# Kernel tuning notes

Measured on AMD Instinct MI355X. Metric: run time of the kernel, lower is better.

Reference implementation:

```python
import jax, jax.numpy as jnp
import numpy as np

NUM_USERS = 100000
NUM_ITEMS = 50000
EMB = 64
B = 8192
MAXM = 50
ATT_H = 16
PRED_H = 8


def setup_inputs() -> dict:
    key = jax.random.key(0)
    ks = jax.random.split(key, 12)
    member_idx = jax.random.randint(ks[0], (B, MAXM), 0, NUM_USERS)
    # ragged group sizes in [1, MAXM]
    lens = jax.random.randint(ks[1], (B,), 1, MAXM + 1)
    member_mask = jnp.arange(MAXM)[None, :] < lens[:, None]  # bool [B, M]
    item_inputs = jax.random.randint(ks[2], (B,), 0, NUM_ITEMS)
    s = 1.0 / np.sqrt(EMB)
    user_table = jax.random.normal(ks[3], (NUM_USERS, EMB), jnp.float32) * s
    item_table = jax.random.normal(ks[4], (NUM_ITEMS, EMB), jnp.float32) * s
    att_w1 = jax.random.normal(ks[5], (2 * EMB, ATT_H), jnp.float32) * 0.05
    att_b1 = jnp.zeros((ATT_H,), jnp.float32)
    att_w2 = jax.random.normal(ks[6], (ATT_H, 1), jnp.float32) * 0.05
    att_b2 = jnp.zeros((1,), jnp.float32)
    pred_w1 = jax.random.normal(ks[7], (3 * EMB, PRED_H), jnp.float32) * 0.05
    pred_b1 = jnp.zeros((PRED_H,), jnp.float32)
    pred_w2 = jax.random.normal(ks[8], (PRED_H, 1), jnp.float32) * 0.05
    pred_b2 = jnp.zeros((1,), jnp.float32)
    return dict(member_idx=member_idx, member_mask=member_mask, item_inputs=item_inputs,
                user_table=user_table, item_table=item_table,
                att_w1=att_w1, att_b1=att_b1, att_w2=att_w2, att_b2=att_b2,
                pred_w1=pred_w1, pred_b1=pred_b1, pred_w2=pred_w2, pred_b2=pred_b2)


def reference(member_idx, member_mask, item_inputs, user_table, item_table,
              att_w1, att_b1, att_w2, att_b2, pred_w1, pred_b1, pred_w2, pred_b2):
    mem_e = user_table[member_idx]            # [B, M, d]
    item_e = item_table[item_inputs]          # [B, d]
    # attention MLP over concat(member, item)
    cat = jnp.concatenate(
        [mem_e, jnp.broadcast_to(item_e[:, None, :], mem_e.shape)], axis=-1)  # [B, M, 2d]
    h = jax.nn.relu(jnp.einsum('bmf,fh->bmh', cat, att_w1) + att_b1)
    logits = (jnp.einsum('bmh,ho->bmo', h, att_w2) + att_b2)[..., 0]          # [B, M]
    logits = jnp.where(member_mask, logits, -jnp.inf)
    wts = jax.nn.softmax(logits, axis=-1)                                     # [B, M]
    g = jnp.einsum('bm,bmd->bd', wts, mem_e)                                  # [B, d]
    new = jnp.concatenate([g * item_e, g, item_e], axis=-1)                   # [B, 3d]
    ph = jax.nn.relu(new @ pred_w1 + pred_b1)
    y = jax.nn.sigmoid(ph @ pred_w2 + pred_b2)                                # [B, 1]
    return y
```

## Files before the change

### kernel.cpp

```cpp
#include <hip/hip_runtime.h>
#include <hip/hip_bf16.h>


__global__ void AGREE_12773232738622_probe(
    const void* member_mask,
    const void* user_table,
    int* ws)
{
    if (ws[2] == 0x5AFE0001) return;

    const int lane = threadIdx.x;
    const int wi = lane >> 4;
    const int r  = lane & 15;

    int len = 0, ok = 1, prev = 1;
    for (int m = 0; m < 50; ++m) {
        long e = 50L * r + m;
        int nz;
        if (wi == 0)      nz = (((const unsigned char*)member_mask)[e] != 0);
        else if (wi == 1) nz = (((const unsigned short*)member_mask)[e] != 0);
        else if (wi == 2) nz = (((const unsigned int*)member_mask)[e] != 0u);
        else {
            const unsigned int* p = (const unsigned int*)member_mask;
            nz = ((p[2 * e] | p[2 * e + 1]) != 0u);
        }
        if (nz && !prev) ok = 0;
        if (nz) len = len + 1;
        prev = nz;
    }
    if (len == 0) ok = 0;

    ok = ok & __shfl_xor(ok, 1);
    ok = ok & __shfl_xor(ok, 2);
    ok = ok & __shfl_xor(ok, 4);
    ok = ok & __shfl_xor(ok, 8);
    int mx = len;
    mx = max(mx, __shfl_xor(mx, 1));
    mx = max(mx, __shfl_xor(mx, 2));
    mx = max(mx, __shfl_xor(mx, 4));
    mx = max(mx, __shfl_xor(mx, 8));

    int o0 = __shfl(ok, 0),  o1 = __shfl(ok, 16), o2 = __shfl(ok, 32), o3 = __shfl(ok, 48);
    int L0 = __shfl(mx, 0),  L1 = __shfl(mx, 16), L2 = __shfl(mx, 32), L3 = __shfl(mx, 48);

    float v = __bfloat162float(((const __hip_bfloat16*)user_table)[lane]);
    float a = (v < 0.0f) ? -v : v;
    int huge = (!(a < 4.0f)) ? 1 : 0;
    unsigned long long hb = __ballot(huge);
    int hcnt = __popcll(hb);

    if (lane == 0) {
        int bestW = 1, bestLen = -1;
        if (o0 && L0 > bestLen) { bestLen = L0; bestW = 1; }
        if (o1 && L1 > bestLen) { bestLen = L1; bestW = 2; }
        if (o2 && L2 > bestLen) { bestLen = L2; bestW = 4; }
        if (o3 && L3 > bestLen) { bestLen = L3; bestW = 8; }
        ws[0] = bestW;
        ws[1] = (hcnt >= 8) ? 1 : 0;
        ws[2] = 0x5AFE0001;
    }
}

__global__ __launch_bounds__(256, 4) void AGREE_12773232738622_kernel(
    const int* member_idx,
    const void* member_mask,
    const int* item_inputs,
    const void* user_table,
    const void* item_table,
    const void* att_w1,
    const void* att_b1,
    const void* att_w2,
    const void* att_b2,
    const void* pred_w1,
    const void* pred_b1,
    const void* pred_w2,
    const void* pred_b2,
    void* out,
    const int* ws)
{
    using s16x8 = __attribute__((ext_vector_type(8))) short;
    using bf16x8 = __attribute__((ext_vector_type(8))) __bf16;
    using f32x4 = __attribute__((ext_vector_type(4))) float;

    __shared__ float s_l[4][64];
    __shared__ float s_g[4][64];

    const int tid  = threadIdx.x;
    const int lane = tid & 63;
    const int wave = tid >> 6;
    const int b    = blockIdx.x * 4 + wave;
    const int mode = ws[0];
    const int isf  = ws[1];

    int valid = 0;
    if (lane < 50) {
        long e0 = 50L * b + lane;
        if (mode == 1)      valid = (((const unsigned char*)member_mask)[e0] != 0);
        else if (mode == 2) valid = (((const unsigned short*)member_mask)[e0] != 0);
        else if (mode == 4) valid = (((const unsigned int*)member_mask)[e0] != 0u);
        else {
            const unsigned int* p = (const unsigned int*)member_mask;
            valid = ((p[2 * e0] | p[2 * e0 + 1]) != 0u);
        }
    }
    unsigned long long vm = __ballot(valid);
    int len = __popcll(vm);
    if (len < 1)  len = 1;
    if (len > 50) len = 50;

    const int item_id = item_inputs[b];
    int idxv = 0;
    if (lane < 50) idxv = member_idx[b * 50 + lane];

    if (!isf) {
        const unsigned short* utp = (const unsigned short*)user_table;
        const unsigned short* w1p = (const unsigned short*)att_w1;

        const float itemv = __uint_as_float(
            (unsigned int)((const unsigned short*)item_table)[item_id * 64 + lane] << 16);

        const int kn = lane & 15;
        const int kg = lane >> 4;
        s16x8 bfrag[4];
        #pragma unroll
        for (int kc = 0; kc < 4; ++kc) {
            #pragma unroll
            for (int j = 0; j < 8; ++j)
                bfrag[kc][j] = (short)w1p[(kc * 32 + kg * 8 + j) * 16 + kn];
        }

        s16x8 afrag[4][2];
        #pragma unroll
        for (int t = 0; t < 4; ++t) {
            int m  = t * 16 + (lane & 15);
            int mc = (m < 50) ? m : 0;
            int id = __shfl(idxv, mc);
            const unsigned short* rp = utp + (long)id * 64 + kg * 8;
            afrag[t][0] = *(const s16x8*)(rp);
            afrag[t][1] = *(const s16x8*)(rp + 32);
        }
        const unsigned short* ipp = (const unsigned short*)item_table + (long)item_id * 64 + kg * 8;
        s16x8 ifrag0 = *(const s16x8*)(ipp);
        s16x8 ifrag1 = *(const s16x8*)(ipp + 32);

        f32x4 acc[4];
        #pragma unroll
        for (int t = 0; t < 4; ++t) acc[t] = f32x4{0.0f, 0.0f, 0.0f, 0.0f};
        #pragma unroll
        for (int t = 0; t < 4; ++t) {
            acc[t] = __builtin_amdgcn_mfma_f32_16x16x32_bf16(
                __builtin_bit_cast(bf16x8, afrag[t][0]), __builtin_bit_cast(bf16x8, bfrag[0]), acc[t], 0, 0, 0);
            acc[t] = __builtin_amdgcn_mfma_f32_16x16x32_bf16(
                __builtin_bit_cast(bf16x8, afrag[t][1]), __builtin_bit_cast(bf16x8, bfrag[1]), acc[t], 0, 0, 0);
            acc[t] = __builtin_amdgcn_mfma_f32_16x16x32_bf16(
                __builtin_bit_cast(bf16x8, ifrag0),     __builtin_bit_cast(bf16x8, bfrag[2]), acc[t], 0, 0, 0);
            acc[t] = __builtin_amdgcn_mfma_f32_16x16x32_bf16(
                __builtin_bit_cast(bf16x8, ifrag1),     __builtin_bit_cast(bf16x8, bfrag[3]), acc[t], 0, 0, 0);
        }

        const float b1v = __uint_as_float((unsigned int)((const unsigned short*)att_b1)[kn] << 16);
        const float w2v = __uint_as_float((unsigned int)((const unsigned short*)att_w2)[kn] << 16);
        const float b2v = __uint_as_float((unsigned int)((const unsigned short*)att_b2)[0] << 16);
        #pragma unroll
        for (int t = 0; t < 4; ++t) {
            #pragma unroll
            for (int r = 0; r < 4; ++r) {
                float v = fmaxf(acc[t][r] + b1v, 0.0f) * w2v;
                v += __shfl_xor(v, 1);
                v += __shfl_xor(v, 2);
                v += __shfl_xor(v, 4);
                v += __shfl_xor(v, 8);
                if ((lane & 15) == 0) s_l[wave][t * 16 + (lane >> 4) * 4 + r] = v;
            }
        }
        __syncthreads();

        float lg = (lane < 50) ? s_l[wave][lane] : 0.0f;

        float x = valid ? (lg + b2v) : -3.0e38f;
        float mxv = x;
        mxv = fmaxf(mxv, __shfl_xor(mxv, 1));
        mxv = fmaxf(mxv, __shfl_xor(mxv, 2));
        mxv = fmaxf(mxv, __shfl_xor(mxv, 4));
        mxv = fmaxf(mxv, __shfl_xor(mxv, 8));
        mxv = fmaxf(mxv, __shfl_xor(mxv, 16));
        mxv = fmaxf(mxv, __shfl_xor(mxv, 32));
        float p = valid ? expf(x - mxv) : 0.0f;
        float sum = p;
        sum += __shfl_xor(sum, 1);
        sum += __shfl_xor(sum, 2);
        sum += __shfl_xor(sum, 4);
        sum += __shfl_xor(sum, 8);
        sum += __shfl_xor(sum, 16);
        sum += __shfl_xor(sum, 32);
        float wnorm;
        if (sum > 0.0f) wnorm = p * (1.0f / sum);
        else            wnorm = (lane == 0) ? 1.0f : 0.0f;

        float pg[2][8];
        #pragma unroll
        for (int ks = 0; ks < 2; ++ks)
            #pragma unroll
            for (int j = 0; j < 8; ++j) pg[ks][j] = 0.0f;
        #pragma unroll
        for (int t = 0; t < 4; ++t) {
            float wv = __shfl(wnorm, t * 16 + (lane & 15));
            #pragma unroll
            for (int ks = 0; ks < 2; ++ks) {
                #pragma unroll
                for (int j = 0; j < 8; ++j) {
                    float e = __uint_as_float(
                        (unsigned int)(unsigned short)afrag[t][ks][j] << 16);
                    pg[ks][j] += wv * e;
                }
            }
        }
        #pragma unroll
        for (int ks = 0; ks < 2; ++ks) {
            #pragma unroll
            for (int j = 0; j < 8; ++j) {
                float v = pg[ks][j];
                v += __shfl_xor(v, 1);
                v += __shfl_xor(v, 2);
                v += __shfl_xor(v, 4);
                v += __shfl_xor(v, 8);
                pg[ks][j] = v;
            }
        }
        if ((lane & 15) == 0) {
            #pragma unroll
            for (int ks = 0; ks < 2; ++ks)
                #pragma unroll
                for (int j = 0; j < 8; ++j)
                    s_g[wave][ks * 32 + (lane >> 4) * 8 + j] = pg[ks][j];
        }
        __syncthreads();
        const float g = s_g[wave][lane];

        const float gi = g * itemv;
        const uint4* pw4 = (const uint4*)pred_w1;
        uint4 A = pw4[lane];
        uint4 Bv = pw4[64 + lane];
        uint4 C = pw4[128 + lane];
        float ea[8], eb[8], ec[8];
        ea[0] = __uint_as_float(A.x << 16);  ea[1] = __uint_as_float(A.x & 0xFFFF0000u);
        ea[2] = __uint_as_float(A.y << 16);  ea[3] = __uint_as_float(A.y & 0xFFFF0000u);
        ea[4] = __uint_as_float(A.z << 16);  ea[5] = __uint_as_float(A.z & 0xFFFF0000u);
        ea[6] = __uint_as_float(A.w << 16);  ea[7] = __uint_as_float(A.w & 0xFFFF0000u);
        eb[0] = __uint_as_float(Bv.x << 16); eb[1] = __uint_as_float(Bv.x & 0xFFFF0000u);
        eb[2] = __uint_as_float(Bv.y << 16); eb[3] = __uint_as_float(Bv.y & 0xFFFF0000u);
        eb[4] = __uint_as_float(Bv.z << 16); eb[5] = __uint_as_float(Bv.z & 0xFFFF0000u);
        eb[6] = __uint_as_float(Bv.w << 16); eb[7] = __uint_as_float(Bv.w & 0xFFFF0000u);
        ec[0] = __uint_as_float(C.x << 16);  ec[1] = __uint_as_float(C.x & 0xFFFF0000u);
        ec[2] = __uint_as_float(C.y << 16);  ec[3] = __uint_as_float(C.y & 0xFFFF0000u);
        ec[4] = __uint_as_float(C.z << 16);  ec[5] = __uint_as_float(C.z & 0xFFFF0000u);
        ec[6] = __uint_as_float(C.w << 16);  ec[7] = __uint_as_float(C.w & 0xFFFF0000u);
        float p8[8];
        #pragma unroll
        for (int k2 = 0; k2 < 8; ++k2)
            p8[k2] = gi * ea[k2] + g * eb[k2] + itemv * ec[k2];
        #pragma unroll
        for (int k2 = 0; k2 < 8; ++k2) {
            float v = p8[k2];
            v += __shfl_xor(v, 1);
            v += __shfl_xor(v, 2);
            v += __shfl_xor(v, 4);
            v += __shfl_xor(v, 8);
            v += __shfl_xor(v, 16);
            v += __shfl_xor(v, 32);
            p8[k2] = v;
        }
        if (lane == 0) {
            float z = __uint_as_float((unsigned int)((const unsigned short*)pred_b2)[0] << 16);
            for (int k2 = 0; k2 < 8; ++k2) {
                float bb2 = __uint_as_float((unsigned int)((const unsigned short*)pred_b1)[k2] << 16);
                float ww  = __uint_as_float((unsigned int)((const unsigned short*)pred_w2)[k2] << 16);
                float hh = p8[k2] + bb2;
                if (hh < 0.0f) hh = 0.0f;
                z += hh * ww;
            }
            float y = 1.0f / (1.0f + expf(-z));
            ((__hip_bfloat16*)out)[b] = __float2bfloat16(y);
        }
    } else {
        const float itemv = ((const float*)item_table)[item_id * 64 + lane];

        float part;
        {
            const int kk = lane & 15;
            const int c  = lane >> 4;
            part = (c == 0) ? ((const float*)att_b1)[kk] : 0.0f;
            for (int t = 0; t < 16; ++t) {
                int f = c * 16 + t;
                float iv = __shfl(itemv, f);
                part += iv * ((const float*)att_w1)[(64 + f) * 16 + kk];
            }
            part += __shfl_xor(part, 16);
            part += __shfl_xor(part, 32);
        }
        float h[16];
        #pragma unroll
        for (int k = 0; k < 16; ++k) h[k] = __shfl(part, k);

        if (lane < len) {
            const float* rp = (const float*)user_table + (long)idxv * 64;
            const float* w1 = (const float*)att_w1;
            #pragma unroll 4
            for (int c = 0; c < 16; ++c) {
                float4 v = ((const float4*)rp)[c];
                #pragma unroll
                for (int k = 0; k < 16; ++k) {
                    h[k] += v.x * w1[(c * 4 + 0) * 16 + k];
                    h[k] += v.y * w1[(c * 4 + 1) * 16 + k];
                    h[k] += v.z * w1[(c * 4 + 2) * 16 + k];
                    h[k] += v.w * w1[(c * 4 + 3) * 16 + k];
                }
            }
        }

        float lg = ((const float*)att_b2)[0];
        #pragma unroll
        for (int k = 0; k < 16; ++k)
            lg += fmaxf(h[k], 0.0f) * ((const float*)att_w2)[k];

        float x = valid ? lg : -3.0e38f;
        float mxv = x;
        mxv = fmaxf(mxv, __shfl_xor(mxv, 1));
        mxv = fmaxf(mxv, __shfl_xor(mxv, 2));
        mxv = fmaxf(mxv, __shfl_xor(mxv, 4));
        mxv = fmaxf(mxv, __shfl_xor(mxv, 8));
        mxv = fmaxf(mxv, __shfl_xor(mxv, 16));
        mxv = fmaxf(mxv, __shfl_xor(mxv, 32));
        float p = valid ? expf(x - mxv) : 0.0f;
        float sum = p;
        sum += __shfl_xor(sum, 1);
        sum += __shfl_xor(sum, 2);
        sum += __shfl_xor(sum, 4);
        sum += __shfl_xor(sum, 8);
        sum += __shfl_xor(sum, 16);
        sum += __shfl_xor(sum, 32);
        float wnorm;
        if (sum > 0.0f) wnorm = p * (1.0f / sum);
        else            wnorm = (lane == 0) ? 1.0f : 0.0f;

        float g = 0.0f;
        const float* ut = (const float*)user_table;
        for (int m = 0; m < len; ++m) {
            int idm  = __shfl(idxv, m);
            float wv = __shfl(wnorm, m);
            g += wv * ut[(long)idm * 64 + lane];
        }

        const float gi = g * itemv;
        const float4* pw4 = (const float4*)pred_w1;
        float4 a0 = pw4[lane * 2],         a1 = pw4[lane * 2 + 1];
        float4 b0 = pw4[(64 + lane) * 2],  b1 = pw4[(64 + lane) * 2 + 1];
        float4 c0 = pw4[(128 + lane) * 2], c1 = pw4[(128 + lane) * 2 + 1];
        float p8[8];
        p8[0] = gi * a0.x + g * b0.x + itemv * c0.x;
        p8[1] = gi * a0.y + g * b0.y + itemv * c0.y;
        p8[2] = gi * a0.z + g * b0.z + itemv * c0.z;
        p8[3] = gi * a0.w + g * b0.w + itemv * c0.w;
        p8[4] = gi * a1.x + g * b1.x + itemv * c1.x;
        p8[5] = gi * a1.y + g * b1.y + itemv * c1.y;
        p8[6] = gi * a1.z + g * b1.z + itemv * c1.z;
        p8[7] = gi * a1.w + g * b1.w + itemv * c1.w;
        #pragma unroll
        for (int k2 = 0; k2 < 8; ++k2) {
            float v = p8[k2];
            v += __shfl_xor(v, 1);
            v += __shfl_xor(v, 2);
            v += __shfl_xor(v, 4);
            v += __shfl_xor(v, 8);
            v += __shfl_xor(v, 16);
            v += __shfl_xor(v, 32);
            p8[k2] = v;
        }
        if (lane == 0) {
            float z = ((const float*)pred_b2)[0];
            for (int k2 = 0; k2 < 8; ++k2) {
                float hh = p8[k2] + ((const float*)pred_b1)[k2];
                if (hh < 0.0f) hh = 0.0f;
                z += hh * ((const float*)pred_w2)[k2];
            }
            float y = 1.0f / (1.0f + expf(-z));
            ((float*)out)[b] = y;
        }
    }
}

extern "C" void kernel_launch(void* const* d_in, const int* in_sizes, int n_in,
                              void* d_out, int out_size, void* d_ws, size_t ws_size,
                              hipStream_t stream) {
    (void)in_sizes; (void)n_in; (void)out_size; (void)ws_size;
    AGREE_12773232738622_probe<<<1, 64, 0, stream>>>(
        d_in[1], d_in[3], (int*)d_ws);
    AGREE_12773232738622_kernel<<<2048, 256, 0, stream>>>(
        (const int*)d_in[0],
        d_in[1],
        (const int*)d_in[2],
        d_in[3],
        d_in[4],
        d_in[5],
        d_in[6],
        d_in[7],
        d_in[8],
        d_in[9],
        d_in[10],
        d_in[11],
        d_in[12],
        d_out,
        (const int*)d_ws);
}
```

Baseline: 159.4 us.

## Process two groups per single-wave block to amortize weight loads

Each 64-thread block now handles two batch rows with one wave instead of four rows with four waves. The att_w1 B-fragments and pred_w1 loads are read once and reused for both groups, and more independent gathers and MFMAs are in flight per wave. The cost is higher register pressure from doubled afrag/acc state, which may lower occupancy (launch bounds now 64,3), plus fewer waves overall.

```diff
diff --git a/kernel.cpp b/kernel.cpp
--- a/kernel.cpp
+++ b/kernel.cpp
@@ -61,7 +61,7 @@
     }
 }
 
-__global__ __launch_bounds__(256, 4) void AGREE_12773232738622_kernel(
+__global__ __launch_bounds__(64, 3) void AGREE_12773232738622_kernel(
     const int* member_idx,
     const void* member_mask,
     const int* item_inputs,
@@ -82,42 +82,56 @@
     using bf16x8 = __attribute__((ext_vector_type(8))) __bf16;
     using f32x4 = __attribute__((ext_vector_type(4))) float;
 
-    __shared__ float s_l[4][64];
-    __shared__ float s_g[4][64];
-
-    const int tid  = threadIdx.x;
-    const int lane = tid & 63;
-    const int wave = tid >> 6;
-    const int b    = blockIdx.x * 4 + wave;
+    __shared__ float s_l[2][64];
+    __shared__ float s_g[2][64];
+
+    const int lane = threadIdx.x;
     const int mode = ws[0];
     const int isf  = ws[1];
 
-    int valid = 0;
-    if (lane < 50) {
-        long e0 = 50L * b + lane;
-        if (mode == 1)      valid = (((const unsigned char*)member_mask)[e0] != 0);
-        else if (mode == 2) valid = (((const unsigned short*)member_mask)[e0] != 0);
-        else if (mode == 4) valid = (((const unsigned int*)member_mask)[e0] != 0u);
-        else {
-            const unsigned int* p = (const unsigned int*)member_mask;
-            valid = ((p[2 * e0] | p[2 * e0 + 1]) != 0u);
-        }
+    int bb[2];
+    bb[0] = blockIdx.x * 2;
+    bb[1] = blockIdx.x * 2 + 1;
+
+    int validv[2], lenv[2];
+    #pragma unroll
+    for (int g = 0; g < 2; ++g) {
+        int valid = 0;
+        if (lane < 50) {
+            long e0 = 50L * bb[g] + lane;
+            if (mode == 1)      valid = (((const unsigned char*)member_mask)[e0] != 0);
+            else if (mode == 2) valid = (((const unsigned short*)member_mask)[e0] != 0);
+            else if (mode == 4) valid = (((const unsigned int*)member_mask)[e0] != 0u);
+            else {
+                const unsigned int* p = (const unsigned int*)member_mask;
+                valid = ((p[2 * e0] | p[2 * e0 + 1]) != 0u);
+            }
+        }
+        validv[g] = valid;
+        unsigned long long vm = __ballot(valid);
+        int len = __popcll(vm);
+        if (len < 1)  len = 1;
+        if (len > 50) len = 50;
+        lenv[g] = len;
     }
-    unsigned long long vm = __ballot(valid);
-    int len = __popcll(vm);
-    if (len < 1)  len = 1;
-    if (len > 50) len = 50;
-
-    const int item_id = item_inputs[b];
-    int idxv = 0;
-    if (lane < 50) idxv = member_idx[b * 50 + lane];
+
+    int item_id[2], idxv[2];
+    #pragma unroll
+    for (int g = 0; g < 2; ++g) {
+        item_id[g] = item_inputs[bb[g]];
+        idxv[g] = 0;
+        if (lane < 50) idxv[g] = member_idx[bb[g] * 50 + lane];
+    }
 
     if (!isf) {
         const unsigned short* utp = (const unsigned short*)user_table;
         const unsigned short* w1p = (const unsigned short*)att_w1;
 
-        const float itemv = __uint_as_float(
-            (unsigned int)((const unsigned short*)item_table)[item_id * 64 + lane] << 16);
+        float itemv[2];
+        #pragma unroll
+        for (int g = 0; g < 2; ++g)
+            itemv[g] = __uint_as_float(
+                (unsigned int)((const unsigned short*)item_table)[item_id[g] * 64 + lane] << 16);
 
         const int kn = lane & 15;
         const int kg = lane >> 4;
@@ -129,115 +143,131 @@
                 bfrag[kc][j] = (short)w1p[(kc * 32 + kg * 8 + j) * 16 + kn];
         }
 
-        s16x8 afrag[4][2];
-        #pragma unroll
-        for (int t = 0; t < 4; ++t) {
-            int m  = t * 16 + (lane & 15);
-            int mc = (m < 50) ? m : 0;
-            int id = __shfl(idxv, mc);
-            const unsigned short* rp = utp + (long)id * 64 + kg * 8;
-            afrag[t][0] = *(const s16x8*)(rp);
-            afrag[t][1] = *(const s16x8*)(rp + 32);
-        }
-        const unsigned short* ipp = (const unsigned short*)item_table + (long)item_id * 64 + kg * 8;
-        s16x8 ifrag0 = *(const s16x8*)(ipp);
-        s16x8 ifrag1 = *(const s16x8*)(ipp + 32);
-
-        f32x4 acc[4];
-        #pragma unroll
-        for (int t = 0; t < 4; ++t) acc[t] = f32x4{0.0f, 0.0f, 0.0f, 0.0f};
-        #pragma unroll
-        for (int t = 0; t < 4; ++t) {
-            acc[t] = __builtin_amdgcn_mfma_f32_16x16x32_bf16(
-                __builtin_bit_cast(bf16x8, afrag[t][0]), __builtin_bit_cast(bf16x8, bfrag[0]), acc[t], 0, 0, 0);
-            acc[t] = __builtin_amdgcn_mfma_f32_16x16x32_bf16(
-                __builtin_bit_cast(bf16x8, afrag[t][1]), __builtin_bit_cast(bf16x8, bfrag[1]), acc[t], 0, 0, 0);
-            acc[t] = __builtin_amdgcn_mfma_f32_16x16x32_bf16(
-                __builtin_bit_cast(bf16x8, ifrag0),     __builtin_bit_cast(bf16x8, bfrag[2]), acc[t], 0, 0, 0);
-            acc[t] = __builtin_amdgcn_mfma_f32_16x16x32_bf16(
-                __builtin_bit_cast(bf16x8, ifrag1),     __builtin_bit_cast(bf16x8, bfrag[3]), acc[t], 0, 0, 0);
+        s16x8 afrag[2][4][2];
+        s16x8 ifr[2][2];
+        #pragma unroll
+        for (int g = 0; g < 2; ++g) {
+            #pragma unroll
+            for (int t = 0; t < 4; ++t) {
+                int m  = t * 16 + (lane & 15);
+                int mc = (m < 50) ? m : 0;
+                int id = __shfl(idxv[g], mc);
+                const unsigned short* rp = utp + (long)id * 64 + kg * 8;
+                afrag[g][t][0] = *(const s16x8*)(rp);
+                afrag[g][t][1] = *(const s16x8*)(rp + 32);
+            }
+            const unsigned short* ipp = (const unsigned short*)item_table
+                                      + (long)item_id[g] * 64 + kg * 8;
+            ifr[g][0] = *(const s16x8*)(ipp);
+            ifr[g][1] = *(const s16x8*)(ipp + 32);
+        }
+
+        f32x4 acc[2][4];
+        #pragma unroll
+        for (int g = 0; g < 2; ++g)
+            #pragma unroll
+            for (int t = 0; t < 4; ++t) acc[g][t] = f32x4{0.0f, 0.0f, 0.0f, 0.0f};
+        #pragma unroll
+        for (int g = 0; g < 2; ++g) {
+            #pragma unroll
+            for (int t = 0; t < 4; ++t) {
+                acc[g][t] = __builtin_amdgcn_mfma_f32_16x16x32_bf16(
+                    __builtin_bit_cast(bf16x8, afrag[g][t][0]), __builtin_bit_cast(bf16x8, bfrag[0]), acc[g][t], 0, 0, 0);
+                acc[g][t] = __builtin_amdgcn_mfma_f32_16x16x32_bf16(
+                    __builtin_bit_cast(bf16x8, afrag[g][t][1]), __builtin_bit_cast(bf16x8, bfrag[1]), acc[g][t], 0, 0, 0);
+                acc[g][t] = __builtin_amdgcn_mfma_f32_16x16x32_bf16(
+                    __builtin_bit_cast(bf16x8, ifr[g][0]),      __builtin_bit_cast(bf16x8, bfrag[2]), acc[g][t], 0, 0, 0);
+                acc[g][t] = __builtin_amdgcn_mfma_f32_16x16x32_bf16(
+                    __builtin_bit_cast(bf16x8, ifr[g][1]),      __builtin_bit_cast(bf16x8, bfrag[3]), acc[g][t], 0, 0, 0);
+            }
         }
 
         const float b1v = __uint_as_float((unsigned int)((const unsigned short*)att_b1)[kn] << 16);
         const float w2v = __uint_as_float((unsigned int)((const unsigned short*)att_w2)[kn] << 16);
         const float b2v = __uint_as_float((unsigned int)((const unsigned short*)att_b2)[0] << 16);
         #pragma unroll
-        for (int t = 0; t < 4; ++t) {
-            #pragma unroll
-            for (int r = 0; r < 4; ++r) {
-                float v = fmaxf(acc[t][r] + b1v, 0.0f) * w2v;
-                v += __shfl_xor(v, 1);
-                v += __shfl_xor(v, 2);
-                v += __shfl_xor(v, 4);
-                v += __shfl_xor(v, 8);
-                if ((lane & 15) == 0) s_l[wave][t * 16 + (lane >> 4) * 4 + r] = v;
+        for (int g = 0; g < 2; ++g) {
+            #pragma unroll
+            for (int t = 0; t < 4; ++t) {
+                #pragma unroll
+                for (int r = 0; r < 4; ++r) {
+                    float v = fmaxf(acc[g][t][r] + b1v, 0.0f) * w2v;
+                    v += __shfl_xor(v, 1);
+                    v += __shfl_xor(v, 2);
+                    v += __shfl_xor(v, 4);
+                    v += __shfl_xor(v, 8);
+                    if ((lane & 15) == 0) s_l[g][t * 16 + (lane >> 4) * 4 + r] = v;
+                }
             }
         }
         __syncthreads();
 
-        float lg = (lane < 50) ? s_l[wave][lane] : 0.0f;
-
-        float x = valid ? (lg + b2v) : -3.0e38f;
-        float mxv = x;
-        mxv = fmaxf(mxv, __shfl_xor(mxv, 1));
-        mxv = fmaxf(mxv, __shfl_xor(mxv, 2));
-        mxv = fmaxf(mxv, __shfl_xor(mxv, 4));
-        mxv = fmaxf(mxv, __shfl_xor(mxv, 8));
-        mxv = fmaxf(mxv, __shfl_xor(mxv, 16));
-        mxv = fmaxf(mxv, __shfl_xor(mxv, 32));
-        float p = valid ? expf(x - mxv) : 0.0f;
-        float sum = p;
-        sum += __shfl_xor(sum, 1);
-        sum += __shfl_xor(sum, 2);
-        sum += __shfl_xor(sum, 4);
-        sum += __shfl_xor(sum, 8);
-        sum += __shfl_xor(sum, 16);
-        sum += __shfl_xor(sum, 32);
-        float wnorm;
-        if (sum > 0.0f) wnorm = p * (1.0f / sum);
-        else            wnorm = (lane == 0) ? 1.0f : 0.0f;
-
-        float pg[2][8];
-        #pragma unroll
-        for (int ks = 0; ks < 2; ++ks)
-            #pragma unroll
-            for (int j = 0; j < 8; ++j) pg[ks][j] = 0.0f;
-        #pragma unroll
-        for (int t = 0; t < 4; ++t) {
-            float wv = __shfl(wnorm, t * 16 + (lane & 15));
+        float wnorm[2];
+        #pragma unroll
+        for (int g = 0; g < 2; ++g) {
+            float lg = (lane < 50) ? s_l[g][lane] : 0.0f;
+            float x = validv[g] ? (lg + b2v) : -3.0e38f;
+            float mxv = x;
+            mxv = fmaxf(mxv, __shfl_xor(mxv, 1));
+            mxv = fmaxf(mxv, __shfl_xor(mxv, 2));
+            mxv = fmaxf(mxv, __shfl_xor(mxv, 4));
+            mxv = fmaxf(mxv, __shfl_xor(mxv, 8));
+            mxv = fmaxf(mxv, __shfl_xor(mxv, 16));
+            mxv = fmaxf(mxv, __shfl_xor(mxv, 32));
+            float p = validv[g] ? expf(x - mxv) : 0.0f;
+            float sum = p;
+            sum += __shfl_xor(sum, 1);
+            sum += __shfl_xor(sum, 2);
+            sum += __shfl_xor(sum, 4);
+            sum += __shfl_xor(sum, 8);
+            sum += __shfl_xor(sum, 16);
+            sum += __shfl_xor(sum, 32);
+            if (sum > 0.0f) wnorm[g] = p * (1.0f / sum);
+            else            wnorm[g] = (lane == 0) ? 1.0f : 0.0f;
+        }
+
+        #pragma unroll
+        for (int g = 0; g < 2; ++g) {
+            float pg[2][8];
+            #pragma unroll
+            for (int ks = 0; ks < 2; ++ks)
+                #pragma unroll
+                for (int j = 0; j < 8; ++j) pg[ks][j] = 0.0f;
+            #pragma unroll
+            for (int t = 0; t < 4; ++t) {
+                float wv = __shfl(wnorm[g], t * 16 + (lane & 15));
+                #pragma unroll
+                for (int ks = 0; ks < 2; ++ks) {
+                    #pragma unroll
+                    for (int j = 0; j < 8; ++j) {
+                        float e = __uint_as_float(
+                            (unsigned int)(unsigned short)afrag[g][t][ks][j] << 16);
+                        pg[ks][j] += wv * e;
+                    }
+                }
+            }
             #pragma unroll
             for (int ks = 0; ks < 2; ++ks) {
                 #pragma unroll
                 for (int j = 0; j < 8; ++j) {
-                    float e = __uint_as_float(
-                        (unsigned int)(unsigned short)afrag[t][ks][j] << 16);
-                    pg[ks][j] += wv * e;
-                }
-            }
-        }
-        #pragma unroll
-        for (int ks = 0; ks < 2; ++ks) {
-            #pragma unroll
-            for (int j = 0; j < 8; ++j) {
-                float v = pg[ks][j];
-                v += __shfl_xor(v, 1);
-                v += __shfl_xor(v, 2);
-                v += __shfl_xor(v, 4);
-                v += __shfl_xor(v, 8);
-                pg[ks][j] = v;
-            }
-        }
-        if ((lane & 15) == 0) {
-            #pragma unroll
-            for (int ks = 0; ks < 2; ++ks)
+                    float v = pg[ks][j];
+                    v += __shfl_xor(v, 1);
+                    v += __shfl_xor(v, 2);
+                    v += __shfl_xor(v, 4);
+                    v += __shfl_xor(v, 8);
+                    pg[ks][j] = v;
+                }
+            }
+            if ((lane & 15) == 0) {
                 #pragma unroll
-                for (int j = 0; j < 8; ++j)
-                    s_g[wave][ks * 32 + (lane >> 4) * 8 + j] = pg[ks][j];
+                for (int ks = 0; ks < 2; ++ks)
+                    #pragma unroll
+                    for (int j = 0; j < 8; ++j)
+                        s_g[g][ks * 32 + (lane >> 4) * 8 + j] = pg[ks][j];
+            }
         }
         __syncthreads();
-        const float g = s_g[wave][lane];
-
-        const float gi = g * itemv;
+
         const uint4* pw4 = (const uint4*)pred_w1;
         uint4 A = pw4[lane];
         uint4 Bv = pw4[64 + lane];
@@ -255,136 +285,148 @@
         ec[2] = __uint_as_float(C.y << 16);  ec[3] = __uint_as_float(C.y & 0xFFFF0000u);
         ec[4] = __uint_as_float(C.z << 16);  ec[5] = __uint_as_float(C.z & 0xFFFF0000u);
         ec[6] = __uint_as_float(C.w << 16);  ec[7] = __uint_as_float(C.w & 0xFFFF0000u);
-        float p8[8];
-        #pragma unroll
-        for (int k2 = 0; k2 < 8; ++k2)
-            p8[k2] = gi * ea[k2] + g * eb[k2] + itemv * ec[k2];
-        #pragma unroll
-        for (int k2 = 0; k2 < 8; ++k2) {
-            float v = p8[k2];
-            v += __shfl_xor(v, 1);
-            v += __shfl_xor(v, 2);
-            v += __shfl_xor(v, 4);
-            v += __shfl_xor(v, 8);
-            v += __shfl_xor(v, 16);
-            v += __shfl_xor(v, 32);
-            p8[k2] = v;
-        }
-        if (lane == 0) {
-            float z = __uint_as_float((unsigned int)((const unsigned short*)pred_b2)[0] << 16);
+
+        #pragma unroll
+        for (int g = 0; g < 2; ++g) {
+            const float gv = s_g[g][lane];
+            const float gi = gv * itemv[g];
+            float p8[8];
+            #pragma unroll
+            for (int k2 = 0; k2 < 8; ++k2)
+                p8[k2] = gi * ea[k2] + gv * eb[k2] + itemv[g] * ec[k2];
+            #pragma unroll
             for (int k2 = 0; k2 < 8; ++k2) {
-                float bb2 = __uint_as_float((unsigned int)((const unsigned short*)pred_b1)[k2] << 16);
-                float ww  = __uint_as_float((unsigned int)((const unsigned short*)pred_w2)[k2] << 16);
-                float hh = p8[k2] + bb2;
-                if (hh < 0.0f) hh = 0.0f;
-                z += hh * ww;
-            }
-            float y = 1.0f / (1.0f + expf(-z));
-            ((__hip_bfloat16*)out)[b] = __float2bfloat16(y);
+                float v = p8[k2];
+                v += __shfl_xor(v, 1);
+                v += __shfl_xor(v, 2);
+                v += __shfl_xor(v, 4);
+                v += __shfl_xor(v, 8);
+                v += __shfl_xor(v, 16);
+                v += __shfl_xor(v, 32);
+                p8[k2] = v;
+            }
+            if (lane == 0) {
+                float z = __uint_as_float((unsigned int)((const unsigned short*)pred_b2)[0] << 16);
+                for (int k2 = 0; k2 < 8; ++k2) {
+                    float bb2 = __uint_as_float((unsigned int)((const unsigned short*)pred_b1)[k2] << 16);
+                    float ww  = __uint_as_float((unsigned int)((const unsigned short*)pred_w2)[k2] << 16);
+                    float hh = p8[k2] + bb2;
+                    if (hh < 0.0f) hh = 0.0f;
+                    z += hh * ww;
+                }
+                float y = 1.0f / (1.0f + expf(-z));
+                ((__hip_bfloat16*)out)[bb[g]] = __float2bfloat16(y);
+            }
         }
     } else {
-        const float itemv = ((const float*)item_table)[item_id * 64 + lane];
-
-        float part;
-        {
-            const int kk = lane & 15;
-            const int c  = lane >> 4;
-            part = (c == 0) ? ((const float*)att_b1)[kk] : 0.0f;
-            for (int t = 0; t < 16; ++t) {
-                int f = c * 16 + t;
-                float iv = __shfl(itemv, f);
-                part += iv * ((const float*)att_w1)[(64 + f) * 16 + kk];
-            }
-            part += __shfl_xor(part, 16);
-            part += __shfl_xor(part, 32);
-        }
-        float h[16];
-        #pragma unroll
-        for (int k = 0; k < 16; ++k) h[k] = __shfl(part, k);
-
-        if (lane < len) {
-            const float* rp = (const float*)user_table + (long)idxv * 64;
-            const float* w1 = (const float*)att_w1;
-            #pragma unroll 4
-            for (int c = 0; c < 16; ++c) {
-                float4 v = ((const float4*)rp)[c];
-                #pragma unroll
-                for (int k = 0; k < 16; ++k) {
-                    h[k] += v.x * w1[(c * 4 + 0) * 16 + k];
-                    h[k] += v.y * w1[(c * 4 + 1) * 16 + k];
-                    h[k] += v.z * w1[(c * 4 + 2) * 16 + k];
-                    h[k] += v.w * w1[(c * 4 + 3) * 16 + k];
-                }
-            }
-        }
-
-        float lg = ((const float*)att_b2)[0];
-        #pragma unroll
-        for (int k = 0; k < 16; ++k)
-            lg += fmaxf(h[k], 0.0f) * ((const float*)att_w2)[k];
-
-        float x = valid ? lg : -3.0e38f;
-        float mxv = x;
-        mxv = fmaxf(mxv, __shfl_xor(mxv, 1));
-        mxv = fmaxf(mxv, __shfl_xor(mxv, 2));
-        mxv = fmaxf(mxv, __shfl_xor(mxv, 4));
-        mxv = fmaxf(mxv, __shfl_xor(mxv, 8));
-        mxv = fmaxf(mxv, __shfl_xor(mxv, 16));
-        mxv = fmaxf(mxv, __shfl_xor(mxv, 32));
-        float p = valid ? expf(x - mxv) : 0.0f;
-        float sum = p;
-        sum += __shfl_xor(sum, 1);
-        sum += __shfl_xor(sum, 2);
-        sum += __shfl_xor(sum, 4);
-        sum += __shfl_xor(sum, 8);
-        sum += __shfl_xor(sum, 16);
-        sum += __shfl_xor(sum, 32);
-        float wnorm;
-        if (sum > 0.0f) wnorm = p * (1.0f / sum);
-        else            wnorm = (lane == 0) ? 1.0f : 0.0f;
-
-        float g = 0.0f;
-        const float* ut = (const float*)user_table;
-        for (int m = 0; m < len; ++m) {
-            int idm  = __shfl(idxv, m);
-            float wv = __shfl(wnorm, m);
-            g += wv * ut[(long)idm * 64 + lane];
-        }
-
-        const float gi = g * itemv;
-        const float4* pw4 = (const float4*)pred_w1;
-        float4 a0 = pw4[lane * 2],         a1 = pw4[lane * 2 + 1];
-        float4 b0 = pw4[(64 + lane) * 2],  b1 = pw4[(64 + lane) * 2 + 1];
-        float4 c0 = pw4[(128 + lane) * 2], c1 = pw4[(128 + lane) * 2 + 1];
-        float p8[8];
-        p8[0] = gi * a0.x + g * b0.x + itemv * c0.x;
-        p8[1] = gi * a0.y + g * b0.y + itemv * c0.y;
-        p8[2] = gi * a0.z + g * b0.z + itemv * c0.z;
-        p8[3] = gi * a0.w + g * b0.w + itemv * c0.w;
-        p8[4] = gi * a1.x + g * b1.x + itemv * c1.x;
-        p8[5] = gi * a1.y + g * b1.y + itemv * c1.y;
-        p8[6] = gi * a1.z + g * b1.z + itemv * c1.z;
-        p8[7] = gi * a1.w + g * b1.w + itemv * c1.w;
-        #pragma unroll
-        for (int k2 = 0; k2 < 8; ++k2) {
-            float v = p8[k2];
-            v += __shfl_xor(v, 1);
-            v += __shfl_xor(v, 2);
-            v += __shfl_xor(v, 4);
-            v += __shfl_xor(v, 8);
-            v += __shfl_xor(v, 16);
-            v += __shfl_xor(v, 32);
-            p8[k2] = v;
-        }
-        if (lane == 0) {
-            float z = ((const float*)pred_b2)[0];
+        for (int gsel = 0; gsel < 2; ++gsel) {
+            const int b = bb[gsel];
+            const int valid = validv[gsel];
+            const int len   = lenv[gsel];
+            const int idxg  = idxv[gsel];
+            const float itemv = ((const float*)item_table)[item_id[gsel] * 64 + lane];
+
+            float part;
+            {
+                const int kk = lane & 15;
+                const int c  = lane >> 4;
+                part = (c == 0) ? ((const float*)att_b1)[kk] : 0.0f;
+                for (int t = 0; t < 16; ++t) {
+                    int f = c * 16 + t;
+                    float iv = __shfl(itemv, f);
+                    part += iv * ((const float*)att_w1)[(64 + f) * 16 + kk];
+                }
+                part += __shfl_xor(part, 16);
+                part += __shfl_xor(part, 32);
+            }
+            float h[16];
+            #pragma unroll
+            for (int k = 0; k < 16; ++k) h[k] = __shfl(part, k);
+
+            if (lane < len) {
+                const float* rp = (const float*)user_table + (long)idxg * 64;
+                const float* w1 = (const float*)att_w1;
+                #pragma unroll 4
+                for (int c = 0; c < 16; ++c) {
+                    float4 v = ((const float4*)rp)[c];
+                    #pragma unroll
+                    for (int k = 0; k < 16; ++k) {
+                        h[k] += v.x * w1[(c * 4 + 0) * 16 + k];
+                        h[k] += v.y * w1[(c * 4 + 1) * 16 + k];
+                        h[k] += v.z * w1[(c * 4 + 2) * 16 + k];
+                        h[k] += v.w * w1[(c * 4 + 3) * 16 + k];
+                    }
+                }
+            }
+
+            float lg = ((const float*)att_b2)[0];
+            #pragma unroll
+            for (int k = 0; k < 16; ++k)
+                lg += fmaxf(h[k], 0.0f) * ((const float*)att_w2)[k];
+
+            float x = valid ? lg : -3.0e38f;
+            float mxv = x;
+            mxv = fmaxf(mxv, __shfl_xor(mxv, 1));
+            mxv = fmaxf(mxv, __shfl_xor(mxv, 2));
+            mxv = fmaxf(mxv, __shfl_xor(mxv, 4));
+            mxv = fmaxf(mxv, __shfl_xor(mxv, 8));
+            mxv = fmaxf(mxv, __shfl_xor(mxv, 16));
+            mxv = fmaxf(mxv, __shfl_xor(mxv, 32));
+            float p = valid ? expf(x - mxv) : 0.0f;
+            float sum = p;
+            sum += __shfl_xor(sum, 1);
+            sum += __shfl_xor(sum, 2);
+            sum += __shfl_xor(sum, 4);
+            sum += __shfl_xor(sum, 8);
+            sum += __shfl_xor(sum, 16);
+            sum += __shfl_xor(sum, 32);
+            float wnorm;
+            if (sum > 0.0f) wnorm = p * (1.0f / sum);
+            else            wnorm = (lane == 0) ? 1.0f : 0.0f;
+
+            float g = 0.0f;
+            const float* ut = (const float*)user_table;
+            for (int m = 0; m < len; ++m) {
+                int idm  = __shfl(idxg, m);
+                float wv = __shfl(wnorm, m);
+                g += wv * ut[(long)idm * 64 + lane];
+            }
+
+            const float gi = g * itemv;
+            const float4* pw4 = (const float4*)pred_w1;
+            float4 a0 = pw4[lane * 2],         a1 = pw4[lane * 2 + 1];
+            float4 b0 = pw4[(64 + lane) * 2],  b1 = pw4[(64 + lane) * 2 + 1];
+            float4 c0 = pw4[(128 + lane) * 2], c1 = pw4[(128 + lane) * 2 + 1];
+            float p8[8];
+            p8[0] = gi * a0.x + g * b0.x + itemv * c0.x;
+            p8[1] = gi * a0.y + g * b0.y + itemv * c0.y;
+            p8[2] = gi * a0.z + g * b0.z + itemv * c0.z;
+            p8[3] = gi * a0.w + g * b0.w + itemv * c0.w;
+            p8[4] = gi * a1.x + g * b1.x + itemv * c1.x;
+            p8[5] = gi * a1.y + g * b1.y + itemv * c1.y;
+            p8[6] = gi * a1.z + g * b1.z + itemv * c1.z;
+            p8[7] = gi * a1.w + g * b1.w + itemv * c1.w;
+            #pragma unroll
             for (int k2 = 0; k2 < 8; ++k2) {
-                float hh = p8[k2] + ((const float*)pred_b1)[k2];
-                if (hh < 0.0f) hh = 0.0f;
-                z += hh * ((const float*)pred_w2)[k2];
-            }
-            float y = 1.0f / (1.0f + expf(-z));
-            ((float*)out)[b] = y;
+                float v = p8[k2];
+                v += __shfl_xor(v, 1);
+                v += __shfl_xor(v, 2);
+                v += __shfl_xor(v, 4);
+                v += __shfl_xor(v, 8);
+                v += __shfl_xor(v, 16);
+                v += __shfl_xor(v, 32);
+                p8[k2] = v;
+            }
+            if (lane == 0) {
+                float z = ((const float*)pred_b2)[0];
+                for (int k2 = 0; k2 < 8; ++k2) {
+                    float hh = p8[k2] + ((const float*)pred_b1)[k2];
+                    if (hh < 0.0f) hh = 0.0f;
+                    z += hh * ((const float*)pred_w2)[k2];
+                }
+                float y = 1.0f / (1.0f + expf(-z));
+                ((float*)out)[b] = y;
+            }
         }
     }
 }
@@ -395,7 +437,7 @@
     (void)in_sizes; (void)n_in; (void)out_size; (void)ws_size;
     AGREE_12773232738622_probe<<<1, 64, 0, stream>>>(
         d_in[1], d_in[3], (int*)d_ws);
-    AGREE_12773232738622_kernel<<<2048, 256, 0, stream>>>(
+    AGREE_12773232738622_kernel<<<4096, 64, 0, stream>>>(
         (const int*)d_in[0],
         d_in[1],
         (const int*)d_in[2],
```

New measurement: 194.8 us. +22.2%, slower.
